# Optimization experiments

Measured on AMD Instinct MI355X. Metric: run time of the kernel, lower is better.

Reference implementation:

```python
import jax, jax.numpy as jnp
import numpy as np

WEIGHT = 1000000.0  # style loss weight


def gram_matrix(y):
    # y: [1, ch, h, w]. Original loops over channels i, taking a circular
    # window of local_ch=ch//2 channels and computing features @ features.T.
    # gram[i,a,b] = <F[(i+a)%ch], F[(i+b)%ch]> , so it is a modular gather of
    # the full ch x ch Gram matrix -- compute that once, then gather.
    b, ch, h, w = y.shape
    local_ch = ch // 2
    feats = y[0].reshape(ch, h * w)                      # [ch, hw]
    g_full = feats @ feats.T                             # [ch, ch]
    idx = (jnp.arange(ch)[:, None] + jnp.arange(local_ch)[None, :]) % ch  # [ch, lch]
    gram = g_full[idx[:, :, None], idx[:, None, :]]      # [ch, lch, lch]
    return gram / (b * local_ch * w * h)


def setup_inputs() -> dict:
    key = jax.random.key(0)
    k1, k2 = jax.random.split(key)
    x = jax.random.normal(k1, (1, 512, 64, 64), dtype=jnp.float32)
    target = jax.random.normal(k2, (512, 256, 256), dtype=jnp.float32)
    return {"x": x, "target": target}


def reference(x, target):
    # StyleLoss.forward with mode='loss', no mask: G = gram(x); loss = MSE(G, target)*weight.
    G = gram_matrix(x)
    loss = jnp.mean((G - target) ** 2) * WEIGHT
    return loss
```

## Files before the change

### kernel.cpp

```cpp
#include <hip/hip_runtime.h>
#include <hip/hip_bf16.h>


typedef __attribute__((ext_vector_type(8))) short bf16x8;
typedef __attribute__((ext_vector_type(4))) float f32x4;

#define CH 512
#define KDIM 4096
#define SPLITK 4
#define LOSS_BLOCKS 2048
#define GPAD 768

#define BM 64
#define BK 64
#define LDT 72

static __device__ inline uint4 cvt8_bf16(float4 a, float4 b) {
    float f[8] = {a.x, a.y, a.z, a.w, b.x, b.y, b.z, b.w};
    union { ushort u[8]; uint4 v; } o;
#pragma unroll
    for (int i = 0; i < 8; ++i) {
        __hip_bfloat16 h = __float2bfloat16(f[i]);
        o.u[i] = *reinterpret_cast<ushort*>(&h);
    }
    return o.v;
}

__global__ __launch_bounds__(256) void gemm_kernel(const float* __restrict__ x,
                                                   float* __restrict__ g_part) {
    __shared__ __hip_bfloat16 a_tile[BM * LDT];
    __shared__ __hip_bfloat16 b_tile[BM * LDT];

    const int bm = blockIdx.x, bn = blockIdx.y, kz = blockIdx.z;
    const int tid  = threadIdx.x;
    const int lane = tid & 63;
    const int w    = tid >> 6;
    const int m    = lane & 15;
    const int q    = lane >> 4;

    const int srow = tid >> 3;
    const int scol = (tid & 7) * 8;

    f32x4 acc[4] = {};

    const int NT = (KDIM / SPLITK) / BK;
    const int k0base = kz * (KDIM / SPLITK);

    const float* arow0 = x + (size_t)(bm * 64 + srow) * KDIM + k0base + scol;
    const float* brow0 = x + (size_t)(bn * 64 + srow) * KDIM + k0base + scol;

    float4 pa[2][2], pb[2][2];
#pragma unroll
    for (int p = 0; p < 2; ++p) {
        const float* ap = arow0 + (size_t)p * 32 * KDIM;
        const float* bp = brow0 + (size_t)p * 32 * KDIM;
        pa[p][0] = *(const float4*)(ap);     pa[p][1] = *(const float4*)(ap + 4);
        pb[p][0] = *(const float4*)(bp);     pb[p][1] = *(const float4*)(bp + 4);
    }

    for (int kt = 0; kt < NT; ++kt) {
        if (kt > 0) __syncthreads();
#pragma unroll
        for (int p = 0; p < 2; ++p) {
            uint4 av = cvt8_bf16(pa[p][0], pa[p][1]);
            uint4 bv = cvt8_bf16(pb[p][0], pb[p][1]);
            uint* ap = (uint*)(a_tile + (srow + p * 32) * LDT + scol);
            ap[0] = av.x; ap[1] = av.y; ap[2] = av.z; ap[3] = av.w;
            uint* bp = (uint*)(b_tile + (srow + p * 32) * LDT + scol);
            bp[0] = bv.x; bp[1] = bv.y; bp[2] = bv.z; bp[3] = bv.w;
        }
        __syncthreads();
        if (kt + 1 < NT) {
            const int ko = (kt + 1) * BK;
#pragma unroll
            for (int p = 0; p < 2; ++p) {
                const float* ap = arow0 + (size_t)p * 32 * KDIM + ko;
                const float* bp = brow0 + (size_t)p * 32 * KDIM + ko;
                pa[p][0] = *(const float4*)(ap);     pa[p][1] = *(const float4*)(ap + 4);
                pb[p][0] = *(const float4*)(bp);     pb[p][1] = *(const float4*)(bp + 4);
            }
        }
#pragma unroll
        for (int ks = 0; ks < 2; ++ks) {
            const int kk = ks * 32 + q * 8;
            bf16x8 afrag = *(const bf16x8*)(a_tile + (w * 16 + m) * LDT + kk);
#pragma unroll
            for (int j = 0; j < 4; ++j) {
                bf16x8 bfrag = *(const bf16x8*)(b_tile + (j * 16 + m) * LDT + kk);
                acc[j] = __builtin_amdgcn_mfma_f32_16x16x32_bf16(afrag, bfrag, acc[j], 0, 0, 0);
            }
        }
    }

    float* gp = g_part + ((size_t)kz << 18);
    const int col = lane & 15;
    const int rq  = (lane >> 4) * 4;
#pragma unroll
    for (int j = 0; j < 4; ++j) {
#pragma unroll
        for (int reg = 0; reg < 4; ++reg) {
            const int rg = bm * 64 + w * 16 + rq + reg;
            const int cg = bn * 64 + j * 16 + col;
            gp[rg * CH + cg] = acc[j][reg];
        }
    }
}

__global__ __launch_bounds__(256) void reduce_pad_kernel(const float* __restrict__ g_part,
                                                         float* __restrict__ g_pad) {
    const float gscale = 1.0f / 1048576.0f;
    int t = blockIdx.x * 256 + threadIdx.x;
    const float4* p = (const float4*)g_part;
    float4 s = p[t];
#pragma unroll
    for (int sl = 1; sl < SPLITK; ++sl) {
        float4 v = p[t + sl * 65536];
        s.x += v.x; s.y += v.y; s.z += v.z; s.w += v.w;
    }
    s.x *= gscale; s.y *= gscale; s.z *= gscale; s.w *= gscale;
    const int row = t >> 7;
    const int c4  = t & 127;
    float4* dst = (float4*)(g_pad + (size_t)row * GPAD);
    dst[c4] = s;
    if (c4 < 64) dst[c4 + 128] = s;
}

__global__ __launch_bounds__(256) void loss_kernel(const float* __restrict__ target,
                                                   const float* __restrict__ g_pad,
                                                   float* __restrict__ partials) {
    const float lscale = 1.0e6f / 33554432.0f;

    const int tid  = threadIdx.x;
    const int lane = tid & 63;
    const int wv   = tid >> 6;
    const int blk  = blockIdx.x;
    const int i    = blk >> 2;

    const float4* t4 = (const float4*)target;
    const float* gbase = g_pad + i + 4 * lane;
    float acc = 0.0f;

#pragma unroll
    for (int j = 0; j < 4; ++j) {
        float4 tv[4];
        float4 gv[4];
#pragma unroll
        for (int k = 0; k < 4; ++k) {
            const int idx4 = blk * 4096 + j * 1024 + k * 256 + tid;
            tv[k] = t4[idx4];
            const int a   = (blk & 3) * 64 + j * 16 + k * 4 + wv;
            const int row = (i + a) & 511;
            __builtin_memcpy(&gv[k], gbase + (size_t)row * GPAD, sizeof(float4));
        }
#pragma unroll
        for (int k = 0; k < 4; ++k) {
            float d0 = gv[k].x - tv[k].x;
            float d1 = gv[k].y - tv[k].y;
            float d2 = gv[k].z - tv[k].z;
            float d3 = gv[k].w - tv[k].w;
            acc += d0 * d0 + d1 * d1 + d2 * d2 + d3 * d3;
        }
    }

#pragma unroll
    for (int off = 32; off > 0; off >>= 1) acc += __shfl_xor(acc, off, 64);
    __shared__ float wsum[4];
    if (lane == 0) wsum[wv] = acc;
    __syncthreads();
    if (tid == 0)
        partials[blk] = (wsum[0] + wsum[1] + wsum[2] + wsum[3]) * lscale;
}

__global__ __launch_bounds__(256) void finish_kernel(const float* __restrict__ partials,
                                                     float* __restrict__ out) {
    const int tid  = threadIdx.x;
    const int lane = tid & 63;
    const int wv   = tid >> 6;
    const float4* p = (const float4*)partials;
    float4 a = p[tid], b = p[tid + 256];
    float s = a.x + a.y + a.z + a.w + b.x + b.y + b.z + b.w;
#pragma unroll
    for (int off = 32; off > 0; off >>= 1) s += __shfl_xor(s, off, 64);
    __shared__ float wsum[4];
    if (lane == 0) wsum[wv] = s;
    __syncthreads();
    if (tid == 0) out[0] = wsum[0] + wsum[1] + wsum[2] + wsum[3];
}

extern "C" void kernel_launch(void* const* d_in, const int* in_sizes, int n_in,
                              void* d_out, int out_size, void* d_ws, size_t ws_size,
                              hipStream_t stream) {
    const float* x      = (const float*)d_in[0];
    const float* target = (const float*)d_in[1];
    float* out = (float*)d_out;

    float* g_part   = (float*)d_ws;
    float* g_pad    = g_part + SPLITK * CH * CH;
    float* partials = g_pad + CH * GPAD;

    gemm_kernel<<<dim3(CH / BM, CH / BM, SPLITK), 256, 0, stream>>>(x, g_part);
    reduce_pad_kernel<<<CH * CH / 4 / 256, 256, 0, stream>>>(g_part, g_pad);
    loss_kernel<<<LOSS_BLOCKS, 256, 0, stream>>>(target, g_pad, partials);
    finish_kernel<<<1, 256, 0, stream>>>(partials, out);
}
```

Before: 212.8 us.

## Expand squared loss algebraically and overlap target reduction with Gram GEMM

The loss sum((G_gather - T)^2) is expanded into sum T^2, a count-weighted sum of G^2, and a cross term -2*G*S1, where S1 accumulates target entries scattered back onto full Gram coordinates. Blocks 256 and up of a single fused launch stream the target and build S1 and the T^2 partials, while the first 256 blocks compute the split-K GEMM. This lets the large target read run alongside the GEMM and replaces the padded gather pass with a small per-cell reduction. In exchange it adds shared-memory scatter work per target element and changes the floating-point summation order.

Measured after the change: 210.9 us. No clear change (-0.9%).

```diff
diff --git a/kernel.cpp b/kernel.cpp
--- a/kernel.cpp
+++ b/kernel.cpp
@@ -8,8 +8,6 @@
 #define CH 512
 #define KDIM 4096
 #define SPLITK 4
-#define LOSS_BLOCKS 2048
-#define GPAD 768
 
 #define BM 64
 #define BK 64
@@ -26,140 +24,168 @@
     return o.v;
 }
 
-__global__ __launch_bounds__(256) void gemm_kernel(const float* __restrict__ x,
-                                                   float* __restrict__ g_part) {
+__global__ __launch_bounds__(256) void fused_main_kernel(const float* __restrict__ x,
+                                                         const float* __restrict__ target,
+                                                         float* __restrict__ g_part,
+                                                         float* __restrict__ S1g,
+                                                         float* __restrict__ t2part) {
     __shared__ __hip_bfloat16 a_tile[BM * LDT];
     __shared__ __hip_bfloat16 b_tile[BM * LDT];
-
-    const int bm = blockIdx.x, bn = blockIdx.y, kz = blockIdx.z;
-    const int tid  = threadIdx.x;
+    __shared__ float wavebuf[4][2][256];
+    __shared__ float comb[4][512];
+    __shared__ float t2w[4];
+
+    const int bid = blockIdx.x;
+    const int tid = threadIdx.x;
     const int lane = tid & 63;
     const int w    = tid >> 6;
-    const int m    = lane & 15;
-    const int q    = lane >> 4;
-
-    const int srow = tid >> 3;
-    const int scol = (tid & 7) * 8;
-
-    f32x4 acc[4] = {};
-
-    const int NT = (KDIM / SPLITK) / BK;
-    const int k0base = kz * (KDIM / SPLITK);
-
-    const float* arow0 = x + (size_t)(bm * 64 + srow) * KDIM + k0base + scol;
-    const float* brow0 = x + (size_t)(bn * 64 + srow) * KDIM + k0base + scol;
-
-    float4 pa[2][2], pb[2][2];
-#pragma unroll
-    for (int p = 0; p < 2; ++p) {
-        const float* ap = arow0 + (size_t)p * 32 * KDIM;
-        const float* bp = brow0 + (size_t)p * 32 * KDIM;
-        pa[p][0] = *(const float4*)(ap);     pa[p][1] = *(const float4*)(ap + 4);
-        pb[p][0] = *(const float4*)(bp);     pb[p][1] = *(const float4*)(bp + 4);
-    }
-
-    for (int kt = 0; kt < NT; ++kt) {
-        if (kt > 0) __syncthreads();
+
+    if (bid < 256) {
+        const int bm = bid & 7, bn = (bid >> 3) & 7, kz = bid >> 6;
+        const int m    = lane & 15;
+        const int q    = lane >> 4;
+        const int srow = tid >> 3;
+        const int scol = (tid & 7) * 8;
+
+        f32x4 acc[4] = {};
+
+        const int NT = (KDIM / SPLITK) / BK;
+        const int k0base = kz * (KDIM / SPLITK);
+
+        const float* arow0 = x + (size_t)(bm * 64 + srow) * KDIM + k0base + scol;
+        const float* brow0 = x + (size_t)(bn * 64 + srow) * KDIM + k0base + scol;
+
+        float4 pa[2][2], pb[2][2];
 #pragma unroll
         for (int p = 0; p < 2; ++p) {
-            uint4 av = cvt8_bf16(pa[p][0], pa[p][1]);
-            uint4 bv = cvt8_bf16(pb[p][0], pb[p][1]);
-            uint* ap = (uint*)(a_tile + (srow + p * 32) * LDT + scol);
-            ap[0] = av.x; ap[1] = av.y; ap[2] = av.z; ap[3] = av.w;
-            uint* bp = (uint*)(b_tile + (srow + p * 32) * LDT + scol);
-            bp[0] = bv.x; bp[1] = bv.y; bp[2] = bv.z; bp[3] = bv.w;
-        }
-        __syncthreads();
-        if (kt + 1 < NT) {
-            const int ko = (kt + 1) * BK;
+            const float* ap = arow0 + (size_t)p * 32 * KDIM;
+            const float* bp = brow0 + (size_t)p * 32 * KDIM;
+            pa[p][0] = *(const float4*)(ap);  pa[p][1] = *(const float4*)(ap + 4);
+            pb[p][0] = *(const float4*)(bp);  pb[p][1] = *(const float4*)(bp + 4);
+        }
+
+        for (int kt = 0; kt < NT; ++kt) {
+            if (kt > 0) __syncthreads();
 #pragma unroll
             for (int p = 0; p < 2; ++p) {
-                const float* ap = arow0 + (size_t)p * 32 * KDIM + ko;
-                const float* bp = brow0 + (size_t)p * 32 * KDIM + ko;
-                pa[p][0] = *(const float4*)(ap);     pa[p][1] = *(const float4*)(ap + 4);
-                pb[p][0] = *(const float4*)(bp);     pb[p][1] = *(const float4*)(bp + 4);
-            }
-        }
-#pragma unroll
-        for (int ks = 0; ks < 2; ++ks) {
-            const int kk = ks * 32 + q * 8;
-            bf16x8 afrag = *(const bf16x8*)(a_tile + (w * 16 + m) * LDT + kk);
-#pragma unroll
-            for (int j = 0; j < 4; ++j) {
-                bf16x8 bfrag = *(const bf16x8*)(b_tile + (j * 16 + m) * LDT + kk);
-                acc[j] = __builtin_amdgcn_mfma_f32_16x16x32_bf16(afrag, bfrag, acc[j], 0, 0, 0);
-            }
-        }
-    }
-
-    float* gp = g_part + ((size_t)kz << 18);
-    const int col = lane & 15;
-    const int rq  = (lane >> 4) * 4;
+                uint4 av = cvt8_bf16(pa[p][0], pa[p][1]);
+                uint4 bv = cvt8_bf16(pb[p][0], pb[p][1]);
+                uint* ap = (uint*)(a_tile + (srow + p * 32) * LDT + scol);
+                ap[0] = av.x; ap[1] = av.y; ap[2] = av.z; ap[3] = av.w;
+                uint* bp = (uint*)(b_tile + (srow + p * 32) * LDT + scol);
+                bp[0] = bv.x; bp[1] = bv.y; bp[2] = bv.z; bp[3] = bv.w;
+            }
+            __syncthreads();
+            if (kt + 1 < NT) {
+                const int ko = (kt + 1) * BK;
+#pragma unroll
+                for (int p = 0; p < 2; ++p) {
+                    const float* ap = arow0 + (size_t)p * 32 * KDIM + ko;
+                    const float* bp = brow0 + (size_t)p * 32 * KDIM + ko;
+                    pa[p][0] = *(const float4*)(ap);  pa[p][1] = *(const float4*)(ap + 4);
+                    pb[p][0] = *(const float4*)(bp);  pb[p][1] = *(const float4*)(bp + 4);
+                }
+            }
+#pragma unroll
+            for (int ks = 0; ks < 2; ++ks) {
+                const int kk = ks * 32 + q * 8;
+                bf16x8 afrag = *(const bf16x8*)(a_tile + (w * 16 + m) * LDT + kk);
+#pragma unroll
+                for (int j = 0; j < 4; ++j) {
+                    bf16x8 bfrag = *(const bf16x8*)(b_tile + (j * 16 + m) * LDT + kk);
+                    acc[j] = __builtin_amdgcn_mfma_f32_16x16x32_bf16(afrag, bfrag, acc[j], 0, 0, 0);
+                }
+            }
+        }
+
+        float* gp = g_part + ((size_t)kz << 18);
+        const int col = lane & 15;
+        const int rq  = (lane >> 4) * 4;
+#pragma unroll
+        for (int j = 0; j < 4; ++j) {
+#pragma unroll
+            for (int reg = 0; reg < 4; ++reg) {
+                const int rg = bm * 64 + w * 16 + rq + reg;
+                const int cg = bn * 64 + j * 16 + col;
+                gp[rg * CH + cg] = acc[j][reg];
+            }
+        }
+        return;
+    }
+
+    const int r = bid - 256;
+    const float4* t4 = (const float4*)target;
+
+    float accv[8] = {};
+    float t2 = 0.0f;
+
+    auto segload = [&](int s) -> float4 {
+        const int a = w * 64 + s;
+        const int i = (r - a) & 511;
+        return t4[i * 16384 + a * 64 + lane];
+    };
+    auto process = [&](float4 v, int s, int p) {
+        const int a = w * 64 + s;
+        const int i = (r - a) & 511;
+        t2 += v.x * v.x + v.y * v.y + v.z * v.z + v.w * v.w;
+        *(float4*)&wavebuf[w][p][lane * 4] = v;
+#pragma unroll
+        for (int k = 0; k < 8; ++k) {
+            const int b = (lane + 64 * k - i) & 511;
+            if (b < 256) accv[k] += wavebuf[w][p][b];
+        }
+    };
+
+    float4 va = segload(0), vb = segload(1);
+    for (int s = 0; s < 64; s += 2) {
+        float4 vn0 = {}, vn1 = {};
+        if (s + 2 < 64) { vn0 = segload(s + 2); vn1 = segload(s + 3); }
+        process(va, s, 0);
+        process(vb, s + 1, 1);
+        va = vn0; vb = vn1;
+    }
+
+#pragma unroll
+    for (int k = 0; k < 8; ++k) comb[w][lane + 64 * k] = accv[k];
+#pragma unroll
+    for (int off = 32; off > 0; off >>= 1) t2 += __shfl_xor(t2, off, 64);
+    if (lane == 0) t2w[w] = t2;
+    __syncthreads();
+    const float s0 = comb[0][tid]       + comb[1][tid]       + comb[2][tid]       + comb[3][tid];
+    const float s1 = comb[0][tid + 256] + comb[1][tid + 256] + comb[2][tid + 256] + comb[3][tid + 256];
+    S1g[r * CH + tid]       = s0;
+    S1g[r * CH + tid + 256] = s1;
+    if (tid == 0) t2part[r] = t2w[0] + t2w[1] + t2w[2] + t2w[3];
+}
+
+__global__ __launch_bounds__(256) void final_partial_kernel(const float* __restrict__ g_part,
+                                                            const float* __restrict__ S1g,
+                                                            float* __restrict__ partial2) {
+    const float gscale = 1.0f / 1048576.0f;
+    const int tid = threadIdx.x, bid = blockIdx.x;
+    const int lane = tid & 63, wv = tid >> 6;
+    const int cell = (bid * 256 + tid) * 4;
+    const int r = cell >> 9, c0 = cell & 511;
+
+    float4 g = *(const float4*)(g_part + cell);
+#pragma unroll
+    for (int sl = 1; sl < SPLITK; ++sl) {
+        float4 v = *(const float4*)(g_part + sl * (CH * CH) + cell);
+        g.x += v.x; g.y += v.y; g.z += v.z; g.w += v.w;
+    }
+    float4 s1 = *(const float4*)(S1g + cell);
+
+    float gg[4] = {g.x, g.y, g.z, g.w};
+    float ss[4] = {s1.x, s1.y, s1.z, s1.w};
+    float acc = 0.0f;
 #pragma unroll
     for (int j = 0; j < 4; ++j) {
-#pragma unroll
-        for (int reg = 0; reg < 4; ++reg) {
-            const int rg = bm * 64 + w * 16 + rq + reg;
-            const int cg = bn * 64 + j * 16 + col;
-            gp[rg * CH + cg] = acc[j][reg];
-        }
-    }
-}
-
-__global__ __launch_bounds__(256) void reduce_pad_kernel(const float* __restrict__ g_part,
-                                                         float* __restrict__ g_pad) {
-    const float gscale = 1.0f / 1048576.0f;
-    int t = blockIdx.x * 256 + threadIdx.x;
-    const float4* p = (const float4*)g_part;
-    float4 s = p[t];
-#pragma unroll
-    for (int sl = 1; sl < SPLITK; ++sl) {
-        float4 v = p[t + sl * 65536];
-        s.x += v.x; s.y += v.y; s.z += v.z; s.w += v.w;
-    }
-    s.x *= gscale; s.y *= gscale; s.z *= gscale; s.w *= gscale;
-    const int row = t >> 7;
-    const int c4  = t & 127;
-    float4* dst = (float4*)(g_pad + (size_t)row * GPAD);
-    dst[c4] = s;
-    if (c4 < 64) dst[c4 + 128] = s;
-}
-
-__global__ __launch_bounds__(256) void loss_kernel(const float* __restrict__ target,
-                                                   const float* __restrict__ g_pad,
-                                                   float* __restrict__ partials) {
-    const float lscale = 1.0e6f / 33554432.0f;
-
-    const int tid  = threadIdx.x;
-    const int lane = tid & 63;
-    const int wv   = tid >> 6;
-    const int blk  = blockIdx.x;
-    const int i    = blk >> 2;
-
-    const float4* t4 = (const float4*)target;
-    const float* gbase = g_pad + i + 4 * lane;
-    float acc = 0.0f;
-
-#pragma unroll
-    for (int j = 0; j < 4; ++j) {
-        float4 tv[4];
-        float4 gv[4];
-#pragma unroll
-        for (int k = 0; k < 4; ++k) {
-            const int idx4 = blk * 4096 + j * 1024 + k * 256 + tid;
-            tv[k] = t4[idx4];
-            const int a   = (blk & 3) * 64 + j * 16 + k * 4 + wv;
-            const int row = (i + a) & 511;
-            __builtin_memcpy(&gv[k], gbase + (size_t)row * GPAD, sizeof(float4));
-        }
-#pragma unroll
-        for (int k = 0; k < 4; ++k) {
-            float d0 = gv[k].x - tv[k].x;
-            float d1 = gv[k].y - tv[k].y;
-            float d2 = gv[k].z - tv[k].z;
-            float d3 = gv[k].w - tv[k].w;
-            acc += d0 * d0 + d1 * d1 + d2 * d2 + d3 * d3;
-        }
+        const int c  = c0 + j;
+        const int d1 = (r - c) & 511;
+        const int d2 = (c - r) & 511;
+        const float n = (float)(256 - (d1 < d2 ? d1 : d2));
+        const float gt = gg[j] * gscale;
+        acc += n * gt * gt - 2.0f * gt * ss[j];
     }
 
 #pragma unroll
@@ -167,24 +193,23 @@
     __shared__ float wsum[4];
     if (lane == 0) wsum[wv] = acc;
     __syncthreads();
-    if (tid == 0)
-        partials[blk] = (wsum[0] + wsum[1] + wsum[2] + wsum[3]) * lscale;
-}
-
-__global__ __launch_bounds__(256) void finish_kernel(const float* __restrict__ partials,
+    if (tid == 0) partial2[bid] = wsum[0] + wsum[1] + wsum[2] + wsum[3];
+}
+
+__global__ __launch_bounds__(256) void finish_kernel(const float* __restrict__ partial2,
+                                                     const float* __restrict__ t2part,
                                                      float* __restrict__ out) {
+    const float lscale = 1.0e6f / 33554432.0f;
     const int tid  = threadIdx.x;
     const int lane = tid & 63;
     const int wv   = tid >> 6;
-    const float4* p = (const float4*)partials;
-    float4 a = p[tid], b = p[tid + 256];
-    float s = a.x + a.y + a.z + a.w + b.x + b.y + b.z + b.w;
+    float s = partial2[tid] + t2part[tid] + t2part[tid + 256];
 #pragma unroll
     for (int off = 32; off > 0; off >>= 1) s += __shfl_xor(s, off, 64);
     __shared__ float wsum[4];
     if (lane == 0) wsum[wv] = s;
     __syncthreads();
-    if (tid == 0) out[0] = wsum[0] + wsum[1] + wsum[2] + wsum[3];
+    if (tid == 0) out[0] = (wsum[0] + wsum[1] + wsum[2] + wsum[3]) * lscale;
 }
 
 extern "C" void kernel_launch(void* const* d_in, const int* in_sizes, int n_in,
@@ -195,11 +220,11 @@
     float* out = (float*)d_out;
 
     float* g_part   = (float*)d_ws;
-    float* g_pad    = g_part + SPLITK * CH * CH;
-    float* partials = g_pad + CH * GPAD;
-
-    gemm_kernel<<<dim3(CH / BM, CH / BM, SPLITK), 256, 0, stream>>>(x, g_part);
-    reduce_pad_kernel<<<CH * CH / 4 / 256, 256, 0, stream>>>(g_part, g_pad);
-    loss_kernel<<<LOSS_BLOCKS, 256, 0, stream>>>(target, g_pad, partials);
-    finish_kernel<<<1, 256, 0, stream>>>(partials, out);
-}
+    float* S1g      = g_part + SPLITK * CH * CH;
+    float* t2part   = S1g + CH * CH;
+    float* partial2 = t2part + CH;
+
+    fused_main_kernel<<<768, 256, 0, stream>>>(x, target, g_part, S1g, t2part);
+    final_partial_kernel<<<256, 256, 0, stream>>>(g_part, S1g, partial2);
+    finish_kernel<<<1, 256, 0, stream>>>(partial2, t2part, out);
+}
```
